# Performance work log

Measured on AMD Instinct MI355X. Metric: run time of the kernel, lower is better.

The kernel has to match this reference:

```python
import jax, jax.numpy as jnp
import numpy as np
from jax import lax

Kx, Ky, E, H = 32000, 32000, 256, 512
Tx, B, Ty = 64, 64, 32


def setup_inputs() -> dict:
    key = jax.random.key(0)
    ks = jax.random.split(key, 24)
    g = lambda k, shape: (jax.random.normal(k, shape, jnp.float32) * 0.05)
    return {
        'inputs': jax.random.randint(ks[0], (Tx, B), 0, Kx),
        'trg_len': Ty,
        'enc_emb': g(ks[1], (Kx, E)),
        'W_ih_f': g(ks[2], (3 * H, E)), 'W_hh_f': g(ks[3], (3 * H, H)),
        'b_ih_f': g(ks[4], (3 * H,)), 'b_hh_f': g(ks[5], (3 * H,)),
        'W_ih_b': g(ks[6], (3 * H, E)), 'W_hh_b': g(ks[7], (3 * H, H)),
        'b_ih_b': g(ks[8], (3 * H,)), 'b_hh_b': g(ks[9], (3 * H,)),
        'W_init': g(ks[10], (H, H)), 'b_init': g(ks[11], (H,)),
        'dec_emb': g(ks[12], (Ky, E)),
        'W_ih_d': g(ks[13], (3 * H, E + 2 * H)), 'W_hh_d': g(ks[14], (3 * H, H)),
        'b_ih_d': g(ks[15], (3 * H,)), 'b_hh_d': g(ks[16], (3 * H,)),
        'W_lsm': g(ks[17], (Ky, 3 * H)), 'b_lsm': g(ks[18], (Ky,)),
        'W_a1': g(ks[19], (H, 3 * H)), 'b_a1': g(ks[20], (H,)),
        'W_a2': g(ks[21], (1, H)), 'b_a2': g(ks[22], (1,)),
    }


def gru_cell(x, h, W_ih, W_hh, b_ih, b_hh):
    # PyTorch GRU math
    gi = x @ W_ih.T + b_ih
    gh = h @ W_hh.T + b_hh
    i_r, i_z, i_n = jnp.split(gi, 3, axis=-1)
    h_r, h_z, h_n = jnp.split(gh, 3, axis=-1)
    r = jax.nn.sigmoid(i_r + h_r)
    z = jax.nn.sigmoid(i_z + h_z)
    n = jnp.tanh(i_n + r * h_n)
    return (1.0 - z) * n + z * h


def reference(inputs, trg_len, enc_emb, W_ih_f, W_hh_f, b_ih_f, b_hh_f,
              W_ih_b, W_hh_b, b_ih_b, b_hh_b, W_init, b_init, dec_emb,
              W_ih_d, W_hh_d, b_ih_d, b_hh_d, W_lsm, b_lsm,
              W_a1, b_a1, W_a2, b_a2):
    Bn = inputs.shape[1]
    embeds = enc_emb[inputs]  # [Tx,B,E]
    h0 = jnp.zeros((Bn, H), jnp.float32)

    def step_f(h, x):
        h2 = gru_cell(x, h, W_ih_f, W_hh_f, b_ih_f, b_hh_f)
        return h2, h2

    def step_b(h, x):
        h2 = gru_cell(x, h, W_ih_b, W_hh_b, b_ih_b, b_hh_b)
        return h2, h2

    _, out_f = lax.scan(step_f, h0, embeds)
    h_b, out_b = lax.scan(step_b, h0, embeds[::-1])
    enc_output = jnp.concatenate([out_f, out_b[::-1]], axis=-1)  # [Tx,B,2H]

    hidden = jnp.tanh(h_b @ W_init.T + b_init)  # [B,H], from hidden[-1] (backward dir)
    tok0 = jnp.ones((Bn,), jnp.int32)

    def dec_step(carry, _):
        tok, h = carry
        # additive attention over Tx (softmax over time axis 0)
        hid_rep = jnp.broadcast_to(h[None], enc_output.shape[:2] + (H,))
        attn_in = jnp.concatenate([hid_rep, enc_output], axis=-1)  # [Tx,B,3H]
        s = jnp.tanh(attn_in @ W_a1.T + b_a1) @ W_a2.T + b_a2  # [Tx,B,1]
        w = jax.nn.softmax(s[..., 0], axis=0)  # [Tx,B]
        context = jnp.einsum('tb,tbh->bh', w, enc_output)  # [B,2H]
        emb = dec_emb[tok]  # [B,E]
        rnn_in = jnp.concatenate([emb, context], axis=-1)  # [B,E+2H]
        h2 = gru_cell(rnn_in, h, W_ih_d, W_hh_d, b_ih_d, b_hh_d)
        logits = jnp.concatenate([h2, context], axis=-1) @ W_lsm.T + b_lsm
        out = jax.nn.log_softmax(logits, axis=-1)  # [B,Ky]
        return (jnp.argmax(out, axis=-1).astype(jnp.int32), h2), out

    _, outputs = lax.scan(dec_step, (tok0, hidden), None, length=trg_len)
    return outputs  # [Ty,B,Ky]
```

## Files before the change

### kernel.cpp

```cpp
#include <hip/hip_runtime.h>
#include <math.h>

#define TX 64
#define BN 64
#define TY 32
#define EE 256
#define HH 512
#define H3 1536
#define KYV 32000

typedef __attribute__((ext_vector_type(8))) short bf16x8;
typedef __attribute__((ext_vector_type(4))) float f32x4;
typedef __attribute__((ext_vector_type(4))) short s16x4;

__device__ __forceinline__ float4 ldf4(const float* p) { return *(const float4*)p; }
__device__ __forceinline__ float sigf(float x) { return 1.f / (1.f + expf(-x)); }

__device__ __forceinline__ short f2bf(float x) {
    unsigned u = __float_as_uint(x);
    unsigned r = (u + 0x7fffu + ((u >> 16) & 1u)) >> 16;
    return (short)r;
}
__device__ __forceinline__ float bf2f(short h) {
    return __uint_as_float(((unsigned)(unsigned short)h) << 16);
}

__device__ __forceinline__ void gload_lds16(const short* g, short* l) {
    __builtin_amdgcn_global_load_lds(
        (const __attribute__((address_space(1))) void*)(g),
        (__attribute__((address_space(3))) void*)(l), 16, 0, 0);
}

__global__ __launch_bounds__(256) void gemm_nt_kernel(
    const float* __restrict__ Abase, const int* __restrict__ gather, int lda,
    const float* __restrict__ Bbase, int ldb, int bofs,
    const float* __restrict__ bias, float* __restrict__ C, int ldc, int K)
{
    __shared__ float As[32][68];
    __shared__ float Bs[32][68];
    const int tid = threadIdx.x;
    const int n0 = blockIdx.x * 64;
    const int m0 = blockIdx.y * 64;
    const int tx = tid & 15, ty = tid >> 4;
    const int li = tid >> 2, lk = (tid & 3) * 8;
    float acc[4][4] = {};
    const float* arow = gather ? (Abase + (size_t)gather[m0 + li] * lda)
                               : (Abase + (size_t)(m0 + li) * lda);
    const float* brow = Bbase + (size_t)(n0 + li) * ldb + bofs;
    for (int kt = 0; kt < K; kt += 32) {
        float4 a0 = ldf4(arow + kt + lk);
        float4 a1 = ldf4(arow + kt + lk + 4);
        float4 b0 = ldf4(brow + kt + lk);
        float4 b1 = ldf4(brow + kt + lk + 4);
        __syncthreads();
        As[lk+0][li]=a0.x; As[lk+1][li]=a0.y; As[lk+2][li]=a0.z; As[lk+3][li]=a0.w;
        As[lk+4][li]=a1.x; As[lk+5][li]=a1.y; As[lk+6][li]=a1.z; As[lk+7][li]=a1.w;
        Bs[lk+0][li]=b0.x; Bs[lk+1][li]=b0.y; Bs[lk+2][li]=b0.z; Bs[lk+3][li]=b0.w;
        Bs[lk+4][li]=b1.x; Bs[lk+5][li]=b1.y; Bs[lk+6][li]=b1.z; Bs[lk+7][li]=b1.w;
        __syncthreads();
        #pragma unroll
        for (int k = 0; k < 32; ++k) {
            float4 av = *(const float4*)&As[k][ty*4];
            float4 bv = *(const float4*)&Bs[k][tx*4];
            acc[0][0] += av.x*bv.x; acc[0][1] += av.x*bv.y; acc[0][2] += av.x*bv.z; acc[0][3] += av.x*bv.w;
            acc[1][0] += av.y*bv.x; acc[1][1] += av.y*bv.y; acc[1][2] += av.y*bv.z; acc[1][3] += av.y*bv.w;
            acc[2][0] += av.z*bv.x; acc[2][1] += av.z*bv.y; acc[2][2] += av.z*bv.z; acc[2][3] += av.z*bv.w;
            acc[3][0] += av.w*bv.x; acc[3][1] += av.w*bv.y; acc[3][2] += av.w*bv.z; acc[3][3] += av.w*bv.w;
        }
    }
    #pragma unroll
    for (int ii = 0; ii < 4; ++ii) {
        int r = m0 + ty*4 + ii;
        #pragma unroll
        for (int jj = 0; jj < 4; ++jj) {
            int c = n0 + tx*4 + jj;
            float v = acc[ii][jj];
            if (bias) v += bias[c];
            C[(size_t)r*ldc + c] = v;
        }
    }
}

__global__ __launch_bounds__(256) void wpack_kernel(
    const float* __restrict__ W, short* __restrict__ pk)
{
    const long id = (long)blockIdx.x*256 + threadIdx.x;
    const long total = (long)500*48*4*64;
    if (id >= total) return;
    const int lane = (int)(id & 63);
    const long r1 = id >> 6;
    const int t = (int)(r1 & 3);
    const long r2 = r1 >> 2;
    const int kt = (int)(r2 % 48);
    const int T  = (int)(r2 / 48);
    const int m = lane & 15, q = lane >> 4;
    const int row = T*64 + t*16 + m;
    const int ks  = kt*32 + q*8;
    const float* src = W + (size_t)row*H3 + ks;
    s16x4 h0, h1, l0, l1;
    {
        float4 v = ldf4(src);
        h0.x = f2bf(v.x); l0.x = f2bf(v.x - bf2f(h0.x));
        h0.y = f2bf(v.y); l0.y = f2bf(v.y - bf2f(h0.y));
        h0.z = f2bf(v.z); l0.z = f2bf(v.z - bf2f(h0.z));
        h0.w = f2bf(v.w); l0.w = f2bf(v.w - bf2f(h0.w));
    }
    {
        float4 v = ldf4(src + 4);
        h1.x = f2bf(v.x); l1.x = f2bf(v.x - bf2f(h1.x));
        h1.y = f2bf(v.y); l1.y = f2bf(v.y - bf2f(h1.y));
        h1.z = f2bf(v.z); l1.z = f2bf(v.z - bf2f(h1.z));
        h1.w = f2bf(v.w); l1.w = f2bf(v.w - bf2f(h1.w));
    }
    const size_t gb = (((size_t)T*48 + kt)*8 + 2*t) * 512;
    s16x4* dh = (s16x4*)(pk + gb + lane*8);
    s16x4* dl = (s16x4*)(pk + gb + 512 + lane*8);
    dh[0] = h0; dh[1] = h1;
    dl[0] = l0; dl[1] = l1;
}

__global__ __launch_bounds__(256) void enc_step_kernel(
    const float* __restrict__ GI_f, const float* __restrict__ GI_b,
    const float* __restrict__ Whh_f, const float* __restrict__ bhh_f,
    const float* __restrict__ Whh_b, const float* __restrict__ bhh_b,
    const float* __restrict__ hf_in, float* __restrict__ hf_out,
    const float* __restrict__ hb_in, float* __restrict__ hb_out,
    float* __restrict__ enc_out, int t)
{
    const int blk = blockIdx.x;
    const int dir = blk >> 7;
    const int r = blk & 127;
    const int cgp = r >> 1;
    const int bh = r & 1;
    const int sub = threadIdx.x >> 5;
    const int b = bh*32 + (threadIdx.x & 31);
    const int col = cgp*8 + sub;

    const float* GI = dir ? GI_b : GI_f;
    const float* W  = dir ? Whh_b : Whh_f;
    const float* bh_v = dir ? bhh_b : bhh_f;
    const float* hin  = dir ? hb_in : hf_in;
    float* hout = dir ? hb_out : hf_out;
    const int tstep = dir ? (TX-1-t) : t;

    const float* hrow = hin + b*HH;
    const float* wr = W + (size_t)col*HH;
    const float* wz = W + (size_t)(HH + col)*HH;
    const float* wn = W + (size_t)(2*HH + col)*HH;
    float ar = 0.f, az = 0.f, an = 0.f;
    for (int k = 0; k < HH; k += 4) {
        float4 hv = ldf4(hrow + k);
        float4 A = ldf4(wr + k), Z = ldf4(wz + k), N = ldf4(wn + k);
        ar += hv.x*A.x + hv.y*A.y + hv.z*A.z + hv.w*A.w;
        az += hv.x*Z.x + hv.y*Z.y + hv.z*Z.z + hv.w*Z.w;
        an += hv.x*N.x + hv.y*N.y + hv.z*N.z + hv.w*N.w;
    }
    size_t gbase = ((size_t)tstep*BN + b) * H3;
    float ir = GI[gbase + col];
    float iz = GI[gbase + HH + col];
    float inn = GI[gbase + 2*HH + col];
    float rr = sigf(ir + ar + bh_v[col]);
    float zz = sigf(iz + az + bh_v[HH + col]);
    float nn = tanhf(inn + rr*(an + bh_v[2*HH + col]));
    float hold = hrow[col];
    float h2 = (1.f - zz)*nn + zz*hold;
    hout[b*HH + col] = h2;
    enc_out[((size_t)tstep*BN + b)*(2*HH) + dir*HH + col] = h2;
}

__global__ __launch_bounds__(256) void dec_init_kernel(
    const float* __restrict__ hbf, const float* __restrict__ Wi,
    const float* __restrict__ bi, float* __restrict__ hdec, int* __restrict__ tok)
{
    const int b = blockIdx.x, tid = threadIdx.x;
    const float* hr = hbf + b*HH;
    for (int n = tid; n < HH; n += 256) {
        float acc = bi[n];
        const float* w = Wi + (size_t)n*HH;
        for (int k = 0; k < HH; k += 4) {
            float4 hv = ldf4(hr + k), wv = ldf4(w + k);
            acc += hv.x*wv.x + hv.y*wv.y + hv.z*wv.z + hv.w*wv.w;
        }
        hdec[b*HH + n] = tanhf(acc);
    }
    if (b == 0 && tid < 64) tok[tid] = 1;
}

__global__ __launch_bounds__(256) void attn_kernel(
    const float* __restrict__ h, const float* __restrict__ P,
    const float* __restrict__ enc, const float* __restrict__ Wa1,
    const float* __restrict__ ba1, const float* __restrict__ Wa2,
    const float* __restrict__ ba2, float* __restrict__ ctx,
    short* __restrict__ Ahi, short* __restrict__ Alo)
{
    __shared__ float hs[HH];
    __shared__ float qsl[HH];
    __shared__ float ssl[TX];
    __shared__ float ww[TX];
    const int b = blockIdx.x, tid = threadIdx.x;
    hs[tid] = h[b*HH + tid];
    hs[tid + 256] = h[b*HH + 256 + tid];
    __syncthreads();
    for (int n = tid; n < HH; n += 256) {
        float acc = ba1[n];
        const float* w = Wa1 + (size_t)n*H3;
        for (int k = 0; k < HH; k += 4) {
            float4 wv = ldf4(w + k);
            acc += hs[k]*wv.x + hs[k+1]*wv.y + hs[k+2]*wv.z + hs[k+3]*wv.w;
        }
        qsl[n] = acc;
    }
    __syncthreads();
    {
        const int t = tid >> 2, part = tid & 3;
        const float* p = P + ((size_t)t*BN + b)*HH + part*128;
        const float* w2 = Wa2 + part*128;
        const float* q = qsl + part*128;
        float acc = 0.f;
        for (int k = 0; k < 128; k += 4) {
            float4 pv = ldf4(p + k), wv = ldf4(w2 + k);
            acc += wv.x*tanhf(q[k+0] + pv.x);
            acc += wv.y*tanhf(q[k+1] + pv.y);
            acc += wv.z*tanhf(q[k+2] + pv.z);
            acc += wv.w*tanhf(q[k+3] + pv.w);
        }
        acc += __shfl_xor(acc, 1);
        acc += __shfl_xor(acc, 2);
        if (part == 0) ssl[t] = acc + ba2[0];
    }
    __syncthreads();
    if (tid < 64) {
        float v = ssl[tid];
        float m = v;
        for (int off = 32; off; off >>= 1) m = fmaxf(m, __shfl_xor(m, off));
        float e = expf(v - m);
        float sm = e;
        for (int off = 32; off; off >>= 1) sm += __shfl_xor(sm, off);
        ww[tid] = e / sm;
    }
    __syncthreads();
    for (int c = tid; c < 2*HH; c += 256) {
        float acc = 0.f;
        #pragma unroll 4
        for (int t2 = 0; t2 < TX; ++t2)
            acc += ww[t2] * enc[((size_t)t2*BN + b)*(2*HH) + c];
        ctx[b*(2*HH) + c] = acc;
        short hi = f2bf(acc);
        Ahi[(size_t)b*H3 + HH + c] = hi;
        Alo[(size_t)b*H3 + HH + c] = f2bf(acc - bf2f(hi));
    }
}

__global__ __launch_bounds__(256) void dec_gru_kernel(
    const float* __restrict__ demb, const int* __restrict__ tok,
    const float* __restrict__ ctx, const float* __restrict__ h,
    const float* __restrict__ Wih, const float* __restrict__ Whh,
    const float* __restrict__ bih, const float* __restrict__ bhh,
    float* __restrict__ hout, short* __restrict__ Ahi, short* __restrict__ Alo)
{
    const int col = blockIdx.x*4 + (threadIdx.x >> 6);
    const int b = threadIdx.x & 63;
    const float* emb = demb + (size_t)tok[b]*EE;
    const float* cr = ctx + b*(2*HH);
    const float* hr = h + b*HH;
    const float* wri = Wih + (size_t)col*1280;
    const float* wzi = Wih + (size_t)(HH + col)*1280;
    const float* wni = Wih + (size_t)(2*HH + col)*1280;
    float ir = 0.f, iz = 0.f, inn = 0.f;
    for (int k = 0; k < EE; k += 4) {
        float4 e = ldf4(emb + k);
        float4 A = ldf4(wri + k), Z = ldf4(wzi + k), N = ldf4(wni + k);
        ir  += e.x*A.x + e.y*A.y + e.z*A.z + e.w*A.w;
        iz  += e.x*Z.x + e.y*Z.y + e.z*Z.z + e.w*Z.w;
        inn += e.x*N.x + e.y*N.y + e.z*N.z + e.w*N.w;
    }
    for (int k = 0; k < 2*HH; k += 4) {
        float4 c = ldf4(cr + k);
        float4 A = ldf4(wri + EE + k), Z = ldf4(wzi + EE + k), N = ldf4(wni + EE + k);
        ir  += c.x*A.x + c.y*A.y + c.z*A.z + c.w*A.w;
        iz  += c.x*Z.x + c.y*Z.y + c.z*Z.z + c.w*Z.w;
        inn += c.x*N.x + c.y*N.y + c.z*N.z + c.w*N.w;
    }
    const float* wrh = Whh + (size_t)col*HH;
    const float* wzh = Whh + (size_t)(HH + col)*HH;
    const float* wnh = Whh + (size_t)(2*HH + col)*HH;
    float hrr = 0.f, hzz = 0.f, hnn = 0.f;
    for (int k = 0; k < HH; k += 4) {
        float4 hv = ldf4(hr + k);
        float4 A = ldf4(wrh + k), Z = ldf4(wzh + k), N = ldf4(wnh + k);
        hrr += hv.x*A.x + hv.y*A.y + hv.z*A.z + hv.w*A.w;
        hzz += hv.x*Z.x + hv.y*Z.y + hv.z*Z.z + hv.w*Z.w;
        hnn += hv.x*N.x + hv.y*N.y + hv.z*N.z + hv.w*N.w;
    }
    float rr = sigf(ir + bih[col] + hrr + bhh[col]);
    float zz = sigf(iz + bih[HH + col] + hzz + bhh[HH + col]);
    float nn = tanhf(inn + bih[2*HH + col] + rr*(hnn + bhh[2*HH + col]));
    float hv0 = hr[col];
    float h2 = (1.f - zz)*nn + zz*hv0;
    hout[b*HH + col] = h2;
    short hi = f2bf(h2);
    Ahi[(size_t)b*H3 + col] = hi;
    Alo[(size_t)b*H3 + col] = f2bf(h2 - bf2f(hi));
}

__global__ __launch_bounds__(256, 4) void logits_lds_kernel(
    const short* __restrict__ Ahi, const short* __restrict__ Alo,
    const short* __restrict__ Wpk, const float* __restrict__ blsm,
    float* __restrict__ outrow)
{
    __shared__ __align__(16) short sbuf[2][4096];
    const int tid = threadIdx.x;
    const int wave = tid >> 6, lane = tid & 63;
    const int T = blockIdx.x;
    const int n0 = T * 64;
    const int m = lane & 15, q = lane >> 4;

    const short* arow_h = Ahi + (size_t)(wave*16 + m)*H3 + q*8;
    const short* arow_l = Alo + (size_t)(wave*16 + m)*H3 + q*8;
    const short* wsrc = Wpk + (size_t)T*48*4096;

    f32x4 acc0 = {0,0,0,0}, acc1 = {0,0,0,0}, acc2 = {0,0,0,0}, acc3 = {0,0,0,0};

    {
        const short* g0 = wsrc + (size_t)(2*wave)*512 + lane*8;
        gload_lds16(g0,       &sbuf[0][(2*wave  )*512]);
        gload_lds16(g0 + 512, &sbuf[0][(2*wave+1)*512]);
    }
    __syncthreads();

    int cur = 0;
    for (int kt = 0; kt < 48; ++kt) {
        if (kt < 47) {
            const short* g0 = wsrc + (size_t)(kt+1)*4096 + (2*wave)*512 + lane*8;
            gload_lds16(g0,       &sbuf[cur^1][(2*wave  )*512]);
            gload_lds16(g0 + 512, &sbuf[cur^1][(2*wave+1)*512]);
        }
        bf16x8 ah = *(const bf16x8*)(arow_h + kt*32);
        bf16x8 al = *(const bf16x8*)(arow_l + kt*32);
        const short* bb = &sbuf[cur][0] + lane*8;
        bf16x8 b0h = *(const bf16x8*)(bb + 0*512);
        bf16x8 b0l = *(const bf16x8*)(bb + 1*512);
        bf16x8 b1h = *(const bf16x8*)(bb + 2*512);
        bf16x8 b1l = *(const bf16x8*)(bb + 3*512);
        bf16x8 b2h = *(const bf16x8*)(bb + 4*512);
        bf16x8 b2l = *(const bf16x8*)(bb + 5*512);
        bf16x8 b3h = *(const bf16x8*)(bb + 6*512);
        bf16x8 b3l = *(const bf16x8*)(bb + 7*512);
        acc0 = __builtin_amdgcn_mfma_f32_16x16x32_bf16(ah, b0h, acc0, 0, 0, 0);
        acc0 = __builtin_amdgcn_mfma_f32_16x16x32_bf16(al, b0h, acc0, 0, 0, 0);
        acc0 = __builtin_amdgcn_mfma_f32_16x16x32_bf16(ah, b0l, acc0, 0, 0, 0);
        acc1 = __builtin_amdgcn_mfma_f32_16x16x32_bf16(ah, b1h, acc1, 0, 0, 0);
        acc1 = __builtin_amdgcn_mfma_f32_16x16x32_bf16(al, b1h, acc1, 0, 0, 0);
        acc1 = __builtin_amdgcn_mfma_f32_16x16x32_bf16(ah, b1l, acc1, 0, 0, 0);
        acc2 = __builtin_amdgcn_mfma_f32_16x16x32_bf16(ah, b2h, acc2, 0, 0, 0);
        acc2 = __builtin_amdgcn_mfma_f32_16x16x32_bf16(al, b2h, acc2, 0, 0, 0);
        acc2 = __builtin_amdgcn_mfma_f32_16x16x32_bf16(ah, b2l, acc2, 0, 0, 0);
        acc3 = __builtin_amdgcn_mfma_f32_16x16x32_bf16(ah, b3h, acc3, 0, 0, 0);
        acc3 = __builtin_amdgcn_mfma_f32_16x16x32_bf16(al, b3h, acc3, 0, 0, 0);
        acc3 = __builtin_amdgcn_mfma_f32_16x16x32_bf16(ah, b3l, acc3, 0, 0, 0);
        __syncthreads();
        cur ^= 1;
    }

    const int row = wave*16 + q*4;
    #pragma unroll
    for (int r = 0; r < 4; ++r) {
        size_t ro = (size_t)(row + r)*KYV;
        outrow[ro + n0 +  0 + m] = acc0[r] + blsm[n0 +  0 + m];
        outrow[ro + n0 + 16 + m] = acc1[r] + blsm[n0 + 16 + m];
        outrow[ro + n0 + 32 + m] = acc2[r] + blsm[n0 + 32 + m];
        outrow[ro + n0 + 48 + m] = acc3[r] + blsm[n0 + 48 + m];
    }
}

__global__ __launch_bounds__(256) void logits_mfma_otf_kernel(
    const short* __restrict__ Ahi, const short* __restrict__ Alo,
    const float* __restrict__ W, const float* __restrict__ blsm,
    float* __restrict__ outrow)
{
    const int wave = threadIdx.x >> 6;
    const int lane = threadIdx.x & 63;
    const int n0 = blockIdx.x * 64;
    const int m = lane & 15;
    const int q = lane >> 4;

    const short* arow_h = Ahi + (size_t)(wave*16 + m)*H3 + q*8;
    const short* arow_l = Alo + (size_t)(wave*16 + m)*H3 + q*8;
    const float* brow = W + (size_t)(n0 + m)*H3 + q*8;

    f32x4 acc[4] = {{0,0,0,0},{0,0,0,0},{0,0,0,0},{0,0,0,0}};
    for (int kt = 0; kt < H3; kt += 32) {
        bf16x8 ah = *(const bf16x8*)(arow_h + kt);
        bf16x8 al = *(const bf16x8*)(arow_l + kt);
        float4 w0[4], w1[4];
        #pragma unroll
        for (int t = 0; t < 4; ++t) {
            const float* bp = brow + (size_t)(16*t)*H3 + kt;
            w0[t] = ldf4(bp);
            w1[t] = ldf4(bp + 4);
        }
        #pragma unroll
        for (int t = 0; t < 4; ++t) {
            float f[8] = {w0[t].x, w0[t].y, w0[t].z, w0[t].w,
                          w1[t].x, w1[t].y, w1[t].z, w1[t].w};
            bf16x8 bh, bl;
            #pragma unroll
            for (int j = 0; j < 8; ++j) {
                unsigned u = __float_as_uint(f[j]);
                unsigned hu = u & 0xffff0000u;
                bh[j] = (short)(hu >> 16);
                bl[j] = f2bf(f[j] - __uint_as_float(hu));
            }
            acc[t] = __builtin_amdgcn_mfma_f32_16x16x32_bf16(ah, bh, acc[t], 0, 0, 0);
            acc[t] = __builtin_amdgcn_mfma_f32_16x16x32_bf16(al, bh, acc[t], 0, 0, 0);
            acc[t] = __builtin_amdgcn_mfma_f32_16x16x32_bf16(ah, bl, acc[t], 0, 0, 0);
        }
    }
    const int row = wave*16 + q*4;
    #pragma unroll
    for (int r = 0; r < 4; ++r) {
        size_t ro = (size_t)(row + r)*KYV;
        outrow[ro + n0 +  0 + m] = acc[0][r] + blsm[n0 +  0 + m];
        outrow[ro + n0 + 16 + m] = acc[1][r] + blsm[n0 + 16 + m];
        outrow[ro + n0 + 32 + m] = acc[2][r] + blsm[n0 + 32 + m];
        outrow[ro + n0 + 48 + m] = acc[3][r] + blsm[n0 + 48 + m];
    }
}

__global__ __launch_bounds__(256) void lse_argmax_sub_kernel(
    float* __restrict__ rows, int* __restrict__ tok)
{
    const int b = blockIdx.x, tid = threadIdx.x;
    float4* row4 = (float4*)(rows + (size_t)b*KYV);
    float m = -1e30f, s = 0.f; int bi = 0;
    for (int i = tid; i < KYV/4; i += 256) {
        float4 v = row4[i];
        if (v.x > m) { s = s*expf(m - v.x) + 1.f; m = v.x; bi = 4*i+0; } else s += expf(v.x - m);
        if (v.y > m) { s = s*expf(m - v.y) + 1.f; m = v.y; bi = 4*i+1; } else s += expf(v.y - m);
        if (v.z > m) { s = s*expf(m - v.z) + 1.f; m = v.z; bi = 4*i+2; } else s += expf(v.z - m);
        if (v.w > m) { s = s*expf(m - v.w) + 1.f; m = v.w; bi = 4*i+3; } else s += expf(v.w - m);
    }
    for (int off = 32; off; off >>= 1) {
        float m2 = __shfl_xor(m, off);
        float s2 = __shfl_xor(s, off);
        int i2 = __shfl_xor(bi, off);
        if (m2 > m || (m2 == m && i2 < bi)) { s = s2 + s*expf(m - m2); m = m2; bi = i2; }
        else s = s + s2*expf(m2 - m);
    }
    __shared__ float ms[4], ssh[4];
    __shared__ int is_[4];
    __shared__ float l_sh;
    const int wid = tid >> 6;
    if ((tid & 63) == 0) { ms[wid] = m; ssh[wid] = s; is_[wid] = bi; }
    __syncthreads();
    if (tid == 0) {
        for (int w = 1; w < 4; ++w) {
            float m2 = ms[w], s2 = ssh[w]; int i2 = is_[w];
            if (m2 > m || (m2 == m && i2 < bi)) { s = s2 + s*expf(m - m2); m = m2; bi = i2; }
            else s = s + s2*expf(m2 - m);
        }
        l_sh = m + logf(s);
        tok[b] = bi;
    }
    __syncthreads();
    const float l = l_sh;
    for (int i = tid; i < KYV/4; i += 256) {
        float4 v = row4[i];
        v.x -= l; v.y -= l; v.z -= l; v.w -= l;
        row4[i] = v;
    }
}

extern "C" void kernel_launch(void* const* d_in, const int* in_sizes, int n_in,
                              void* d_out, int out_size, void* d_ws, size_t ws_size,
                              hipStream_t stream)
{
    const int*   inputs  = (const int*)  d_in[0];
    const float* enc_emb = (const float*)d_in[2];
    const float* W_ih_f  = (const float*)d_in[3];
    const float* W_hh_f  = (const float*)d_in[4];
    const float* b_ih_f  = (const float*)d_in[5];
    const float* b_hh_f  = (const float*)d_in[6];
    const float* W_ih_b  = (const float*)d_in[7];
    const float* W_hh_b  = (const float*)d_in[8];
    const float* b_ih_b  = (const float*)d_in[9];
    const float* b_hh_b  = (const float*)d_in[10];
    const float* W_init  = (const float*)d_in[11];
    const float* b_init  = (const float*)d_in[12];
    const float* dec_emb = (const float*)d_in[13];
    const float* W_ih_d  = (const float*)d_in[14];
    const float* W_hh_d  = (const float*)d_in[15];
    const float* b_ih_d  = (const float*)d_in[16];
    const float* b_hh_d  = (const float*)d_in[17];
    const float* W_lsm   = (const float*)d_in[18];
    const float* b_lsm   = (const float*)d_in[19];
    const float* W_a1    = (const float*)d_in[20];
    const float* b_a1    = (const float*)d_in[21];
    const float* W_a2    = (const float*)d_in[22];
    const float* b_a2    = (const float*)d_in[23];

    float* ws = (float*)d_ws;
    float* GI_f   = ws;
    float* GI_b   = GI_f + (size_t)4096*1536;
    float* enc_out= GI_b + (size_t)4096*1536;
    float* P_enc  = enc_out + (size_t)4096*1024;
    float* hf     = P_enc + (size_t)4096*512;
    float* hb     = hf + 2*BN*HH;
    float* hdec   = hb + 2*BN*HH;
    float* ctx    = hdec + 2*BN*HH;
    float* lse    = ctx + BN*2*HH;
    int*   tok    = (int*)(lse + 64);
    short* A_hi = (short*)(tok + 64);
    short* A_lo = A_hi + (size_t)BN*H3;
    short* W_pk = A_lo + (size_t)BN*H3;
    size_t need_bytes = (size_t)((char*)(W_pk + (size_t)KYV*H3*2) - (char*)d_ws);
    const bool packed = (ws_size >= need_bytes);

    hipMemsetAsync(hf, 0, BN*HH*sizeof(float), stream);
    hipMemsetAsync(hb, 0, BN*HH*sizeof(float), stream);

    dim3 g1(H3/64, (TX*BN)/64);
    gemm_nt_kernel<<<g1, 256, 0, stream>>>(enc_emb, inputs, EE, W_ih_f, EE, 0,
                                           b_ih_f, GI_f, H3, EE);
    gemm_nt_kernel<<<g1, 256, 0, stream>>>(enc_emb, inputs, EE, W_ih_b, EE, 0,
                                           b_ih_b, GI_b, H3, EE);

    if (packed) {
        wpack_kernel<<<24000, 256, 0, stream>>>(W_lsm, W_pk);
    }

    for (int t = 0; t < TX; ++t) {
        const float* hfi = hf + (t & 1)*BN*HH;
        float*       hfo = hf + ((t + 1) & 1)*BN*HH;
        const float* hbi = hb + (t & 1)*BN*HH;
        float*       hbo = hb + ((t + 1) & 1)*BN*HH;
        enc_step_kernel<<<256, 256, 0, stream>>>(GI_f, GI_b, W_hh_f, b_hh_f,
                                                 W_hh_b, b_hh_b, hfi, hfo,
                                                 hbi, hbo, enc_out, t);
    }

    dim3 g2(HH/64, (TX*BN)/64);
    gemm_nt_kernel<<<g2, 256, 0, stream>>>(enc_out, nullptr, 2*HH, W_a1, H3, HH,
                                           nullptr, P_enc, HH, 2*HH);

    dec_init_kernel<<<BN, 256, 0, stream>>>(hb, W_init, b_init, hdec, tok);

    float* out = (float*)d_out;
    for (int s = 0; s < TY; ++s) {
        float* h_cur = hdec + (s & 1)*BN*HH;
        float* h_nxt = hdec + ((s + 1) & 1)*BN*HH;
        attn_kernel<<<BN, 256, 0, stream>>>(h_cur, P_enc, enc_out, W_a1, b_a1,
                                            W_a2, b_a2, ctx, A_hi, A_lo);
        dec_gru_kernel<<<128, 256, 0, stream>>>(dec_emb, tok, ctx, h_cur,
                                                W_ih_d, W_hh_d, b_ih_d, b_hh_d,
                                                h_nxt, A_hi, A_lo);
        float* lrow = out + (size_t)s*BN*KYV;
        if (packed) {
            logits_lds_kernel<<<KYV/64, 256, 0, stream>>>(A_hi, A_lo, W_pk,
                                                          b_lsm, lrow);
        } else {
            logits_mfma_otf_kernel<<<KYV/64, 256, 0, stream>>>(A_hi, A_lo, W_lsm,
                                                               b_lsm, lrow);
        }
        lse_argmax_sub_kernel<<<BN, 256, 0, stream>>>(lrow, tok);
    }
}
```

Measured before the change: 10.94 ms.

## Fuse lse/argmax with next-step attention; register-prefetch logits GEMM without LDS

Merges the per-step log-softmax/argmax kernel with the following step's attention kernel into one launch, split by block index, so the two independent pieces run concurrently and one launch per step is removed. Rewrites the logits MFMA kernel to prefetch the next K-tile of A and packed weights straight into registers instead of double-buffering through LDS, which drops the per-iteration barriers. The logits kernel's launch bounds go from 4 to 2, which may lower occupancy and exposes global-load latency without the LDS staging.

```diff
diff --git a/kernel.cpp b/kernel.cpp
--- a/kernel.cpp
+++ b/kernel.cpp
@@ -23,12 +23,6 @@
 }
 __device__ __forceinline__ float bf2f(short h) {
     return __uint_as_float(((unsigned)(unsigned short)h) << 16);
-}
-
-__device__ __forceinline__ void gload_lds16(const short* g, short* l) {
-    __builtin_amdgcn_global_load_lds(
-        (const __attribute__((address_space(1))) void*)(g),
-        (__attribute__((address_space(3))) void*)(l), 16, 0, 0);
 }
 
 __global__ __launch_bounds__(256) void gemm_nt_kernel(
@@ -186,18 +180,14 @@
     if (b == 0 && tid < 64) tok[tid] = 1;
 }
 
-__global__ __launch_bounds__(256) void attn_kernel(
+__device__ __forceinline__ void attn_body(
     const float* __restrict__ h, const float* __restrict__ P,
     const float* __restrict__ enc, const float* __restrict__ Wa1,
     const float* __restrict__ ba1, const float* __restrict__ Wa2,
     const float* __restrict__ ba2, float* __restrict__ ctx,
-    short* __restrict__ Ahi, short* __restrict__ Alo)
-{
-    __shared__ float hs[HH];
-    __shared__ float qsl[HH];
-    __shared__ float ssl[TX];
-    __shared__ float ww[TX];
-    const int b = blockIdx.x, tid = threadIdx.x;
+    short* __restrict__ Ahi, short* __restrict__ Alo,
+    int b, int tid, float* hs, float* qsl, float* ssl, float* ww)
+{
     hs[tid] = h[b*HH + tid];
     hs[tid + 256] = h[b*HH + 256 + tid];
     __syncthreads();
@@ -248,6 +238,71 @@
         short hi = f2bf(acc);
         Ahi[(size_t)b*H3 + HH + c] = hi;
         Alo[(size_t)b*H3 + HH + c] = f2bf(acc - bf2f(hi));
+    }
+}
+
+__device__ __forceinline__ void lse_body(
+    float* __restrict__ rows, int* __restrict__ tok, int b, int tid,
+    float* ms, float* ssh, int* is_, float* l_sh)
+{
+    float4* row4 = (float4*)(rows + (size_t)b*KYV);
+    float m = -1e30f, s = 0.f; int bi = 0;
+    for (int i = tid; i < KYV/4; i += 256) {
+        float4 v = row4[i];
+        if (v.x > m) { s = s*expf(m - v.x) + 1.f; m = v.x; bi = 4*i+0; } else s += expf(v.x - m);
+        if (v.y > m) { s = s*expf(m - v.y) + 1.f; m = v.y; bi = 4*i+1; } else s += expf(v.y - m);
+        if (v.z > m) { s = s*expf(m - v.z) + 1.f; m = v.z; bi = 4*i+2; } else s += expf(v.z - m);
+        if (v.w > m) { s = s*expf(m - v.w) + 1.f; m = v.w; bi = 4*i+3; } else s += expf(v.w - m);
+    }
+    for (int off = 32; off; off >>= 1) {
+        float m2 = __shfl_xor(m, off);
+        float s2 = __shfl_xor(s, off);
+        int i2 = __shfl_xor(bi, off);
+        if (m2 > m || (m2 == m && i2 < bi)) { s = s2 + s*expf(m - m2); m = m2; bi = i2; }
+        else s = s + s2*expf(m2 - m);
+    }
+    const int wid = tid >> 6;
+    if ((tid & 63) == 0) { ms[wid] = m; ssh[wid] = s; is_[wid] = bi; }
+    __syncthreads();
+    if (tid == 0) {
+        for (int w = 1; w < 4; ++w) {
+            float m2 = ms[w], s2 = ssh[w]; int i2 = is_[w];
+            if (m2 > m || (m2 == m && i2 < bi)) { s = s2 + s*expf(m - m2); m = m2; bi = i2; }
+            else s = s + s2*expf(m2 - m);
+        }
+        *l_sh = m + logf(s);
+        tok[b] = bi;
+    }
+    __syncthreads();
+    const float l = *l_sh;
+    for (int i = tid; i < KYV/4; i += 256) {
+        float4 v = row4[i];
+        v.x -= l; v.y -= l; v.z -= l; v.w -= l;
+        row4[i] = v;
+    }
+}
+
+__global__ __launch_bounds__(256) void lse_attn_kernel(
+    float* __restrict__ rows, int* __restrict__ tok,
+    const float* __restrict__ h, const float* __restrict__ P,
+    const float* __restrict__ enc, const float* __restrict__ Wa1,
+    const float* __restrict__ ba1, const float* __restrict__ Wa2,
+    const float* __restrict__ ba2, float* __restrict__ ctx,
+    short* __restrict__ Ahi, short* __restrict__ Alo, int nlse)
+{
+    __shared__ float hs[HH];
+    __shared__ float qsl[HH];
+    __shared__ float ssl[TX];
+    __shared__ float ww[TX];
+    __shared__ float ms[4], ssh[4];
+    __shared__ int is_[4];
+    __shared__ float l_sh;
+    const int B = blockIdx.x, tid = threadIdx.x;
+    if (B < nlse) {
+        lse_body(rows, tok, B, tid, ms, ssh, is_, &l_sh);
+    } else {
+        attn_body(h, P, enc, Wa1, ba1, Wa2, ba2, ctx, Ahi, Alo,
+                  B - nlse, tid, hs, qsl, ssl, ww);
     }
 }
 
@@ -303,12 +358,11 @@
     Alo[(size_t)b*H3 + col] = f2bf(h2 - bf2f(hi));
 }
 
-__global__ __launch_bounds__(256, 4) void logits_lds_kernel(
+__global__ __launch_bounds__(256, 2) void logits_pipe_kernel(
     const short* __restrict__ Ahi, const short* __restrict__ Alo,
     const short* __restrict__ Wpk, const float* __restrict__ blsm,
     float* __restrict__ outrow)
 {
-    __shared__ __align__(16) short sbuf[2][4096];
     const int tid = threadIdx.x;
     const int wave = tid >> 6, lane = tid & 63;
     const int T = blockIdx.x;
@@ -317,50 +371,64 @@
 
     const short* arow_h = Ahi + (size_t)(wave*16 + m)*H3 + q*8;
     const short* arow_l = Alo + (size_t)(wave*16 + m)*H3 + q*8;
-    const short* wsrc = Wpk + (size_t)T*48*4096;
+    const short* wbase = Wpk + (size_t)T*48*4096 + lane*8;
+
+    bf16x8 cah  = *(const bf16x8*)(arow_h);
+    bf16x8 cal  = *(const bf16x8*)(arow_l);
+    bf16x8 cb0h = *(const bf16x8*)(wbase + 0*512);
+    bf16x8 cb0l = *(const bf16x8*)(wbase + 1*512);
+    bf16x8 cb1h = *(const bf16x8*)(wbase + 2*512);
+    bf16x8 cb1l = *(const bf16x8*)(wbase + 3*512);
+    bf16x8 cb2h = *(const bf16x8*)(wbase + 4*512);
+    bf16x8 cb2l = *(const bf16x8*)(wbase + 5*512);
+    bf16x8 cb3h = *(const bf16x8*)(wbase + 6*512);
+    bf16x8 cb3l = *(const bf16x8*)(wbase + 7*512);
 
     f32x4 acc0 = {0,0,0,0}, acc1 = {0,0,0,0}, acc2 = {0,0,0,0}, acc3 = {0,0,0,0};
 
-    {
-        const short* g0 = wsrc + (size_t)(2*wave)*512 + lane*8;
-        gload_lds16(g0,       &sbuf[0][(2*wave  )*512]);
-        gload_lds16(g0 + 512, &sbuf[0][(2*wave+1)*512]);
-    }
-    __syncthreads();
-
-    int cur = 0;
-    for (int kt = 0; kt < 48; ++kt) {
-        if (kt < 47) {
-            const short* g0 = wsrc + (size_t)(kt+1)*4096 + (2*wave)*512 + lane*8;
-            gload_lds16(g0,       &sbuf[cur^1][(2*wave  )*512]);
-            gload_lds16(g0 + 512, &sbuf[cur^1][(2*wave+1)*512]);
-        }
-        bf16x8 ah = *(const bf16x8*)(arow_h + kt*32);
-        bf16x8 al = *(const bf16x8*)(arow_l + kt*32);
-        const short* bb = &sbuf[cur][0] + lane*8;
-        bf16x8 b0h = *(const bf16x8*)(bb + 0*512);
-        bf16x8 b0l = *(const bf16x8*)(bb + 1*512);
-        bf16x8 b1h = *(const bf16x8*)(bb + 2*512);
-        bf16x8 b1l = *(const bf16x8*)(bb + 3*512);
-        bf16x8 b2h = *(const bf16x8*)(bb + 4*512);
-        bf16x8 b2l = *(const bf16x8*)(bb + 5*512);
-        bf16x8 b3h = *(const bf16x8*)(bb + 6*512);
-        bf16x8 b3l = *(const bf16x8*)(bb + 7*512);
-        acc0 = __builtin_amdgcn_mfma_f32_16x16x32_bf16(ah, b0h, acc0, 0, 0, 0);
-        acc0 = __builtin_amdgcn_mfma_f32_16x16x32_bf16(al, b0h, acc0, 0, 0, 0);
-        acc0 = __builtin_amdgcn_mfma_f32_16x16x32_bf16(ah, b0l, acc0, 0, 0, 0);
-        acc1 = __builtin_amdgcn_mfma_f32_16x16x32_bf16(ah, b1h, acc1, 0, 0, 0);
-        acc1 = __builtin_amdgcn_mfma_f32_16x16x32_bf16(al, b1h, acc1, 0, 0, 0);
-        acc1 = __builtin_amdgcn_mfma_f32_16x16x32_bf16(ah, b1l, acc1, 0, 0, 0);
-        acc2 = __builtin_amdgcn_mfma_f32_16x16x32_bf16(ah, b2h, acc2, 0, 0, 0);
-        acc2 = __builtin_amdgcn_mfma_f32_16x16x32_bf16(al, b2h, acc2, 0, 0, 0);
-        acc2 = __builtin_amdgcn_mfma_f32_16x16x32_bf16(ah, b2l, acc2, 0, 0, 0);
-        acc3 = __builtin_amdgcn_mfma_f32_16x16x32_bf16(ah, b3h, acc3, 0, 0, 0);
-        acc3 = __builtin_amdgcn_mfma_f32_16x16x32_bf16(al, b3h, acc3, 0, 0, 0);
-        acc3 = __builtin_amdgcn_mfma_f32_16x16x32_bf16(ah, b3l, acc3, 0, 0, 0);
-        __syncthreads();
-        cur ^= 1;
-    }
+    #pragma unroll 2
+    for (int kt = 0; kt < 47; ++kt) {
+        const short* wn = wbase + (size_t)(kt+1)*4096;
+        bf16x8 nah  = *(const bf16x8*)(arow_h + (kt+1)*32);
+        bf16x8 nal  = *(const bf16x8*)(arow_l + (kt+1)*32);
+        bf16x8 nb0h = *(const bf16x8*)(wn + 0*512);
+        bf16x8 nb0l = *(const bf16x8*)(wn + 1*512);
+        bf16x8 nb1h = *(const bf16x8*)(wn + 2*512);
+        bf16x8 nb1l = *(const bf16x8*)(wn + 3*512);
+        bf16x8 nb2h = *(const bf16x8*)(wn + 4*512);
+        bf16x8 nb2l = *(const bf16x8*)(wn + 5*512);
+        bf16x8 nb3h = *(const bf16x8*)(wn + 6*512);
+        bf16x8 nb3l = *(const bf16x8*)(wn + 7*512);
+
+        acc0 = __builtin_amdgcn_mfma_f32_16x16x32_bf16(cah, cb0h, acc0, 0, 0, 0);
+        acc0 = __builtin_amdgcn_mfma_f32_16x16x32_bf16(cal, cb0h, acc0, 0, 0, 0);
+        acc0 = __builtin_amdgcn_mfma_f32_16x16x32_bf16(cah, cb0l, acc0, 0, 0, 0);
+        acc1 = __builtin_amdgcn_mfma_f32_16x16x32_bf16(cah, cb1h, acc1, 0, 0, 0);
+        acc1 = __builtin_amdgcn_mfma_f32_16x16x32_bf16(cal, cb1h, acc1, 0, 0, 0);
+        acc1 = __builtin_amdgcn_mfma_f32_16x16x32_bf16(cah, cb1l, acc1, 0, 0, 0);
+        acc2 = __builtin_amdgcn_mfma_f32_16x16x32_bf16(cah, cb2h, acc2, 0, 0, 0);
+        acc2 = __builtin_amdgcn_mfma_f32_16x16x32_bf16(cal, cb2h, acc2, 0, 0, 0);
+        acc2 = __builtin_amdgcn_mfma_f32_16x16x32_bf16(cah, cb2l, acc2, 0, 0, 0);
+        acc3 = __builtin_amdgcn_mfma_f32_16x16x32_bf16(cah, cb3h, acc3, 0, 0, 0);
+        acc3 = __builtin_amdgcn_mfma_f32_16x16x32_bf16(cal, cb3h, acc3, 0, 0, 0);
+        acc3 = __builtin_amdgcn_mfma_f32_16x16x32_bf16(cah, cb3l, acc3, 0, 0, 0);
+
+        cah = nah; cal = nal;
+        cb0h = nb0h; cb0l = nb0l; cb1h = nb1h; cb1l = nb1l;
+        cb2h = nb2h; cb2l = nb2l; cb3h = nb3h; cb3l = nb3l;
+    }
+    acc0 = __builtin_amdgcn_mfma_f32_16x16x32_bf16(cah, cb0h, acc0, 0, 0, 0);
+    acc0 = __builtin_amdgcn_mfma_f32_16x16x32_bf16(cal, cb0h, acc0, 0, 0, 0);
+    acc0 = __builtin_amdgcn_mfma_f32_16x16x32_bf16(cah, cb0l, acc0, 0, 0, 0);
+    acc1 = __builtin_amdgcn_mfma_f32_16x16x32_bf16(cah, cb1h, acc1, 0, 0, 0);
+    acc1 = __builtin_amdgcn_mfma_f32_16x16x32_bf16(cal, cb1h, acc1, 0, 0, 0);
+    acc1 = __builtin_amdgcn_mfma_f32_16x16x32_bf16(cah, cb1l, acc1, 0, 0, 0);
+    acc2 = __builtin_amdgcn_mfma_f32_16x16x32_bf16(cah, cb2h, acc2, 0, 0, 0);
+    acc2 = __builtin_amdgcn_mfma_f32_16x16x32_bf16(cal, cb2h, acc2, 0, 0, 0);
+    acc2 = __builtin_amdgcn_mfma_f32_16x16x32_bf16(cah, cb2l, acc2, 0, 0, 0);
+    acc3 = __builtin_amdgcn_mfma_f32_16x16x32_bf16(cah, cb3h, acc3, 0, 0, 0);
+    acc3 = __builtin_amdgcn_mfma_f32_16x16x32_bf16(cal, cb3h, acc3, 0, 0, 0);
+    acc3 = __builtin_amdgcn_mfma_f32_16x16x32_bf16(cah, cb3l, acc3, 0, 0, 0);
 
     const int row = wave*16 + q*4;
     #pragma unroll
@@ -424,50 +492,6 @@
         outrow[ro + n0 + 16 + m] = acc[1][r] + blsm[n0 + 16 + m];
         outrow[ro + n0 + 32 + m] = acc[2][r] + blsm[n0 + 32 + m];
         outrow[ro + n0 + 48 + m] = acc[3][r] + blsm[n0 + 48 + m];
-    }
-}
-
-__global__ __launch_bounds__(256) void lse_argmax_sub_kernel(
-    float* __restrict__ rows, int* __restrict__ tok)
-{
-    const int b = blockIdx.x, tid = threadIdx.x;
-    float4* row4 = (float4*)(rows + (size_t)b*KYV);
-    float m = -1e30f, s = 0.f; int bi = 0;
-    for (int i = tid; i < KYV/4; i += 256) {
-        float4 v = row4[i];
-        if (v.x > m) { s = s*expf(m - v.x) + 1.f; m = v.x; bi = 4*i+0; } else s += expf(v.x - m);
-        if (v.y > m) { s = s*expf(m - v.y) + 1.f; m = v.y; bi = 4*i+1; } else s += expf(v.y - m);
-        if (v.z > m) { s = s*expf(m - v.z) + 1.f; m = v.z; bi = 4*i+2; } else s += expf(v.z - m);
-        if (v.w > m) { s = s*expf(m - v.w) + 1.f; m = v.w; bi = 4*i+3; } else s += expf(v.w - m);
-    }
-    for (int off = 32; off; off >>= 1) {
-        float m2 = __shfl_xor(m, off);
-        float s2 = __shfl_xor(s, off);
-        int i2 = __shfl_xor(bi, off);
-        if (m2 > m || (m2 == m && i2 < bi)) { s = s2 + s*expf(m - m2); m = m2; bi = i2; }
-        else s = s + s2*expf(m2 - m);
-    }
-    __shared__ float ms[4], ssh[4];
-    __shared__ int is_[4];
-    __shared__ float l_sh;
-    const int wid = tid >> 6;
-    if ((tid & 63) == 0) { ms[wid] = m; ssh[wid] = s; is_[wid] = bi; }
-    __syncthreads();
-    if (tid == 0) {
-        for (int w = 1; w < 4; ++w) {
-            float m2 = ms[w], s2 = ssh[w]; int i2 = is_[w];
-            if (m2 > m || (m2 == m && i2 < bi)) { s = s2 + s*expf(m - m2); m = m2; bi = i2; }
-            else s = s + s2*expf(m2 - m);
-        }
-        l_sh = m + logf(s);
-        tok[b] = bi;
-    }
-    __syncthreads();
-    const float l = l_sh;
-    for (int i = tid; i < KYV/4; i += 256) {
-        float4 v = row4[i];
-        v.x -= l; v.y -= l; v.z -= l; v.w -= l;
-        row4[i] = v;
     }
 }
 
@@ -546,22 +570,34 @@
     dec_init_kernel<<<BN, 256, 0, stream>>>(hb, W_init, b_init, hdec, tok);
 
     float* out = (float*)d_out;
+
+    lse_attn_kernel<<<64, 256, 0, stream>>>(out, tok, hdec, P_enc, enc_out,
+                                            W_a1, b_a1, W_a2, b_a2, ctx,
+                                            A_hi, A_lo, 0);
     for (int s = 0; s < TY; ++s) {
         float* h_cur = hdec + (s & 1)*BN*HH;
         float* h_nxt = hdec + ((s + 1) & 1)*BN*HH;
-        attn_kernel<<<BN, 256, 0, stream>>>(h_cur, P_enc, enc_out, W_a1, b_a1,
-                                            W_a2, b_a2, ctx, A_hi, A_lo);
         dec_gru_kernel<<<128, 256, 0, stream>>>(dec_emb, tok, ctx, h_cur,
                                                 W_ih_d, W_hh_d, b_ih_d, b_hh_d,
                                                 h_nxt, A_hi, A_lo);
         float* lrow = out + (size_t)s*BN*KYV;
         if (packed) {
-            logits_lds_kernel<<<KYV/64, 256, 0, stream>>>(A_hi, A_lo, W_pk,
-                                                          b_lsm, lrow);
+            logits_pipe_kernel<<<KYV/64, 256, 0, stream>>>(A_hi, A_lo, W_pk,
+                                                           b_lsm, lrow);
         } else {
             logits_mfma_otf_kernel<<<KYV/64, 256, 0, stream>>>(A_hi, A_lo, W_lsm,
                                                                b_lsm, lrow);
         }
-        lse_argmax_sub_kernel<<<BN, 256, 0, stream>>>(lrow, tok);
-    }
-}
+        if (s < TY-1) {
+            lse_attn_kernel<<<128, 256, 0, stream>>>(lrow, tok, h_nxt, P_enc,
+                                                     enc_out, W_a1, b_a1,
+                                                     W_a2, b_a2, ctx,
+                                                     A_hi, A_lo, 64);
+        } else {
+            lse_attn_kernel<<<64, 256, 0, stream>>>(lrow, tok, h_nxt, P_enc,
+                                                    enc_out, W_a1, b_a1,
+                                                    W_a2, b_a2, ctx,
+                                                    A_hi, A_lo, 64);
+        }
+    }
+}
```

After: 10.14 ms. 1.08x faster.
